# Kernel optimization log

Hardware: AMD Instinct MI355X
Metric: run time of the kernel (lower is better)

## Reference

```python
import jax, jax.numpy as jnp
import numpy as np

N_NODES = 100000
N_EDGES = 1600000
D_IN = 128
D_HID = 128
N_LAYERS = 3


def setup_inputs() -> dict:
    key = jax.random.key(0)
    k1, k2, k3, k4 = jax.random.split(key, 4)
    x = jax.random.normal(k1, (N_NODES, D_IN), dtype=jnp.float32)
    edge_index = jax.random.randint(k2, (2, N_EDGES), 0, N_NODES, dtype=jnp.int64)
    # Glorot-ish scale for stability across 3 layers
    Ws = jax.random.normal(k3, (N_LAYERS, D_IN, D_HID), dtype=jnp.float32) * (1.0 / np.sqrt(D_IN))
    bs = jax.random.normal(k4, (N_LAYERS, D_HID), dtype=jnp.float32) * 0.01
    return {"x": x, "edge_index": edge_index, "Ws": Ws, "bs": bs}


def _gcn_conv(x, row, col, deg_inv_sqrt, W, b, n_nodes):
    # Linear transform first (PyG GCNConv), then gather-normalize-scatter.
    h = x @ W                                        # [N, D]
    norm = deg_inv_sqrt[row] * deg_inv_sqrt[col]     # [E+N] (self-loops included)
    msg = h[row] * norm[:, None]                     # gather + scale, [E+N, D]
    out = jax.ops.segment_sum(msg, col, num_segments=n_nodes)  # scatter-add
    return out + b


def reference(x, edge_index, Ws, bs):
    n = x.shape[0]
    # add self-loops once (same for every layer)
    loop = jnp.arange(n, dtype=edge_index.dtype)
    row = jnp.concatenate([edge_index[0], loop])
    col = jnp.concatenate([edge_index[1], loop])
    # symmetric normalization: deg over target nodes (incl. self-loops)
    deg = jax.ops.segment_sum(jnp.ones_like(col, dtype=x.dtype), col, num_segments=n)
    deg_inv_sqrt = jnp.where(deg > 0, jax.lax.rsqrt(jnp.maximum(deg, 1.0)), 0.0)
    h = x
    for i in range(Ws.shape[0]):
        h = jax.nn.relu(_gcn_conv(h, row, col, deg_inv_sqrt, Ws[i], bs[i], n))
    return h
```

## Files before the change

### kernel.cpp

```cpp
#include <hip/hip_runtime.h>
#include <hip/hip_bf16.h>

#define NN 100000
#define NROWS 100032
#define NE 1600000
#define DD 128
#define NBUK 196
#define F1_BLOCKS 256
#define F3_BLOCKS 256

typedef unsigned short ushort_t;
typedef unsigned int uint_t;
typedef __attribute__((ext_vector_type(8))) short bf16x8;
typedef __attribute__((ext_vector_type(4))) float f32x4;

__device__ __forceinline__ ushort_t bf16rne(float f) {
    uint_t u = __float_as_uint(f);
    u += 0x7FFF + ((u >> 16) & 1);
    return (ushort_t)(u >> 16);
}
__device__ __forceinline__ float bfLo(uint_t u) { return __uint_as_float(u << 16); }
__device__ __forceinline__ float bfHi(uint_t u) { return __uint_as_float(u & 0xFFFF0000u); }


__global__ __launch_bounds__(256) void f1_bucket_count(const int* __restrict__ col,
                                                       int* __restrict__ bukCount) {
    __shared__ int hist[NBUK];
    for (int t = threadIdx.x; t < NBUK; t += 256) hist[t] = 0;
    __syncthreads();
    const int epb = (NE + F1_BLOCKS - 1) / F1_BLOCKS;
    const int e0 = blockIdx.x * epb;
    const int e1 = min(e0 + epb, NE);
    for (int e = e0 + threadIdx.x; e < e1; e += 256)
        atomicAdd(&hist[col[e] >> 9], 1);
    __syncthreads();
    for (int t = threadIdx.x; t < NBUK; t += 256)
        if (hist[t]) atomicAdd(&bukCount[t], hist[t]);
}

__global__ void f2_bucket_scan(const int* __restrict__ bukCount,
                               int* __restrict__ bukBase,
                               int* __restrict__ bukCursor,
                               int* __restrict__ offsets) {
    __shared__ int s[256];
    const int t = threadIdx.x;
    int v = (t < NBUK) ? bukCount[t] : 0;
    s[t] = v;
    __syncthreads();
    for (int off = 1; off < 256; off <<= 1) {
        int tmp = (t >= off) ? s[t - off] : 0;
        __syncthreads();
        s[t] += tmp;
        __syncthreads();
    }
    int excl = s[t] - v;
    if (t < NBUK) { bukBase[t] = excl; bukCursor[t] = excl; }
    if (t == 255) { bukBase[NBUK] = s[255]; offsets[NN] = s[255]; }
}

__global__ __launch_bounds__(256) void f3_scatter(const int* __restrict__ row,
                                                  const int* __restrict__ col,
                                                  int* __restrict__ bukCursor,
                                                  int* __restrict__ ebuf) {
    __shared__ int hist[4][NBUK];
    __shared__ int base[4][NBUK];
    const int t = threadIdx.x;
    const int w = t >> 6;
    const int lane = t & 63;
    for (int i = t; i < 4 * NBUK; i += 256) (&hist[0][0])[i] = 0;
    __syncthreads();
    const int epb = (NE + F3_BLOCKS - 1) / F3_BLOCKS;
    const int e0 = blockIdx.x * epb;
    const int e1 = min(e0 + epb, NE);
    const int wepb = (e1 - e0 + 3) >> 2;
    const int we0 = e0 + w * wepb;
    const int we1 = min(we0 + wepb, e1);
    for (int e = we0 + lane; e < we1; e += 64)
        atomicAdd(&hist[w][col[e] >> 9], 1);
    __syncthreads();
    if (t < NBUK) {
        int h0 = hist[0][t], h1 = hist[1][t], h2 = hist[2][t], h3 = hist[3][t];
        int tot = h0 + h1 + h2 + h3;
        int g = tot ? atomicAdd(&bukCursor[t], tot) : 0;
        base[0][t] = g; base[1][t] = g + h0;
        base[2][t] = g + h0 + h1; base[3][t] = g + h0 + h1 + h2;
        hist[0][t] = 0; hist[1][t] = 0; hist[2][t] = 0; hist[3][t] = 0;
    }
    __syncthreads();
    for (int e = we0 + lane; e < we1; e += 64) {
        int c = col[e];
        int b = c >> 9;
        int r = atomicAdd(&hist[w][b], 1);
        ebuf[base[w][b] + r] = (row[e] << 9) | (c & 511);
    }
}

__global__ __launch_bounds__(256) void f4_finalize(const int* __restrict__ ebuf,
                                                   const int* __restrict__ bukBase,
                                                   int* __restrict__ offsets,
                                                   float* __restrict__ dis,
                                                   int* __restrict__ csr_src) {
    __shared__ int cnt[512];
    __shared__ int cur[512];
    __shared__ int s[256];
    const int t = threadIdx.x;
    const int colBase = blockIdx.x << 9;
    const int ncols = min(512, NN - colBase);
    cnt[t] = 0; cnt[t + 256] = 0;
    __syncthreads();
    const int eb0 = bukBase[blockIdx.x];
    const int eb1 = bukBase[blockIdx.x + 1];
    for (int e = eb0 + t; e < eb1; e += 256)
        atomicAdd(&cnt[ebuf[e] & 511], 1);
    __syncthreads();
    const int c0 = cnt[2 * t], c1 = cnt[2 * t + 1];
    const int psum = c0 + c1;
    s[t] = psum;
    __syncthreads();
    for (int off = 1; off < 256; off <<= 1) {
        int tmp = (t >= off) ? s[t - off] : 0;
        __syncthreads();
        s[t] += tmp;
        __syncthreads();
    }
    const int exclPair = s[t] - psum;
    const int g0 = eb0 + exclPair;
    const int g1 = g0 + c0;
    cur[2 * t] = g0; cur[2 * t + 1] = g1;
    if (2 * t < ncols)     { offsets[colBase + 2 * t]     = g0; dis[colBase + 2 * t]     = rsqrtf((float)(c0 + 1)); }
    if (2 * t + 1 < ncols) { offsets[colBase + 2 * t + 1] = g1; dis[colBase + 2 * t + 1] = rsqrtf((float)(c1 + 1)); }
    __syncthreads();
    for (int e = eb0 + t; e < eb1; e += 256) {
        int pc = ebuf[e];
        int p = atomicAdd(&cur[pc & 511], 1);
        csr_src[p] = pc >> 9;
    }
}


__global__ __launch_bounds__(256) void wt_kernel(const float* __restrict__ Ws,
                                                 ushort_t* __restrict__ wT) {
    int idx = blockIdx.x * 256 + threadIdx.x;
    if (idx >= 3 * 128 * 16) return;
    int l = idx >> 11;
    int r = idx & 2047;
    int c = r >> 4;
    int kc = r & 15;
    const float* w = Ws + l * 16384;
    ushort_t tmp[8];
#pragma unroll
    for (int e = 0; e < 8; ++e)
        tmp[e] = bf16rne(w[(kc * 8 + e) * 128 + c]);
    *(uint4*)&wT[(size_t)l * 16384 + c * 128 + kc * 8] = *(uint4*)tmp;
}


template<bool XF32>
__global__ __launch_bounds__(256) void gemm_mfma(const void* __restrict__ Xv,
                                                 const ushort_t* __restrict__ wT,
                                                 const float* __restrict__ dis,
                                                 ushort_t* __restrict__ Y) {
    __shared__ short smem[128 * 136];
    {
        const uint4* src = (const uint4*)wT;
        int t = threadIdx.x;
#pragma unroll
        for (int i = 0; i < 8; ++i) {
            int idx = i * 256 + t;
            int rowc = idx >> 4;
            int kc = idx & 15;
            uint4 v = src[idx];
            *(uint4*)&smem[rowc * 136 + kc * 8] = v;
        }
    }
    __syncthreads();

    const int wave = threadIdx.x >> 6;
    const int lane = threadIdx.x & 63;
    const int m = lane & 15;
    const int kg = lane >> 4;
    const int r0 = blockIdx.x * 64 + wave * 16;
    const int rowA = min(r0 + m, NN - 1);

    f32x4 acc[8];
#pragma unroll
    for (int ct = 0; ct < 8; ++ct) acc[ct] = (f32x4){0.f, 0.f, 0.f, 0.f};

#pragma unroll
    for (int ks = 0; ks < 4; ++ks) {
        bf16x8 af;
        if (XF32) {
            const float* xp = (const float*)Xv + (size_t)rowA * DD + ks * 32 + kg * 8;
            float4 f0 = *(const float4*)xp;
            float4 f1 = *(const float4*)(xp + 4);
            af[0] = (short)bf16rne(f0.x); af[1] = (short)bf16rne(f0.y);
            af[2] = (short)bf16rne(f0.z); af[3] = (short)bf16rne(f0.w);
            af[4] = (short)bf16rne(f1.x); af[5] = (short)bf16rne(f1.y);
            af[6] = (short)bf16rne(f1.z); af[7] = (short)bf16rne(f1.w);
        } else {
            const ushort_t* xp = (const ushort_t*)Xv + (size_t)rowA * DD + ks * 32 + kg * 8;
            af = *(const bf16x8*)xp;
        }
#pragma unroll
        for (int ct = 0; ct < 8; ++ct) {
            bf16x8 bf = *(const bf16x8*)&smem[(ct * 16 + m) * 136 + ks * 32 + kg * 8];
            acc[ct] = __builtin_amdgcn_mfma_f32_16x16x32_bf16(af, bf, acc[ct], 0, 0, 0);
        }
    }

    __syncthreads();

    ushort_t* sl = (ushort_t*)smem;
    const int rbase = r0 + kg * 4;
    float dv[4];
#pragma unroll
    for (int rg = 0; rg < 4; ++rg) dv[rg] = dis[min(rbase + rg, NN - 1)];
#pragma unroll
    for (int ct = 0; ct < 8; ++ct) {
#pragma unroll
        for (int rg = 0; rg < 4; ++rg)
            sl[(wave * 16 + kg * 4 + rg) * 132 + ct * 16 + m] = bf16rne(acc[ct][rg] * dv[rg]);
    }

    const int lr = lane >> 2;
    const int q  = lane & 3;
    const int grow = r0 + lr;
    const ushort_t* rb = sl + (wave * 16 + lr) * 132 + q * 32;
    uint2 d0 = *(const uint2*)(rb + 0);
    uint2 d1 = *(const uint2*)(rb + 4);
    uint2 d2 = *(const uint2*)(rb + 8);
    uint2 d3 = *(const uint2*)(rb + 12);
    uint2 d4 = *(const uint2*)(rb + 16);
    uint2 d5 = *(const uint2*)(rb + 20);
    uint2 d6 = *(const uint2*)(rb + 24);
    uint2 d7 = *(const uint2*)(rb + 28);
    const bool ok = grow < NN;
    uint4 v0 = ok ? make_uint4(d0.x, d0.y, d1.x, d1.y) : make_uint4(0, 0, 0, 0);
    uint4 v1 = ok ? make_uint4(d2.x, d2.y, d3.x, d3.y) : make_uint4(0, 0, 0, 0);
    uint4 v2 = ok ? make_uint4(d4.x, d4.y, d5.x, d5.y) : make_uint4(0, 0, 0, 0);
    uint4 v3 = ok ? make_uint4(d6.x, d6.y, d7.x, d7.y) : make_uint4(0, 0, 0, 0);
    uint4* yp = (uint4*)&Y[(size_t)grow * DD + q * 32];
    yp[0] = v0; yp[1] = v1; yp[2] = v2; yp[3] = v3;
}


template<bool F32OUT>
__global__ __launch_bounds__(256) void agg_kernel(const uint_t* __restrict__ lin2,
                                                  const int* __restrict__ offsets,
                                                  const int* __restrict__ csr_src,
                                                  const float* __restrict__ dis,
                                                  const float* __restrict__ bias,
                                                  void* __restrict__ outv) {
    const int bid = blockIdx.x;
    const int xcd = bid & 7;
    const int h   = (xcd >> 2);
    const int g   = (bid >> 3) * 4 + (xcd & 3);
    const int w    = threadIdx.x >> 6;
    const int lane = threadIdx.x & 63;
    const int l32  = lane & 31;
    const int hi   = lane >> 5;
    const int v = g * 8 + w * 2 + hi;

    const int start = offsets[v];
    const int end   = offsets[v + 1];
    const int n     = end - start;
    const int nvm   = n < 32 ? n : 32;

    int idxv = NN;
    if (l32 < nvm) idxv = csr_src[start + l32];

    const int nv_other = __shfl(nvm, lane ^ 32);
    int kmax = nvm > nv_other ? nvm : nv_other;
    kmax = (kmax + 7) & ~7;

    const uint_t doff = (uint_t)(h * 32 + l32);
    const float dv = dis[v];
    uint_t self = lin2[((uint_t)v << 6) | doff];
    float2 b    = ((const float2*)bias)[doff];

    float accx = 0.f, accy = 0.f;
    const int sbase = (lane & 32);
    for (int k = 0; k < kmax; k += 8) {
        int s0 = __shfl(idxv, sbase + k + 0);
        int s1 = __shfl(idxv, sbase + k + 1);
        int s2 = __shfl(idxv, sbase + k + 2);
        int s3 = __shfl(idxv, sbase + k + 3);
        int s4 = __shfl(idxv, sbase + k + 4);
        int s5 = __shfl(idxv, sbase + k + 5);
        int s6 = __shfl(idxv, sbase + k + 6);
        int s7 = __shfl(idxv, sbase + k + 7);
        uint_t a0 = lin2[((uint_t)s0 << 6) | doff];
        uint_t a1 = lin2[((uint_t)s1 << 6) | doff];
        uint_t a2 = lin2[((uint_t)s2 << 6) | doff];
        uint_t a3 = lin2[((uint_t)s3 << 6) | doff];
        uint_t a4 = lin2[((uint_t)s4 << 6) | doff];
        uint_t a5 = lin2[((uint_t)s5 << 6) | doff];
        uint_t a6 = lin2[((uint_t)s6 << 6) | doff];
        uint_t a7 = lin2[((uint_t)s7 << 6) | doff];
        accx += bfLo(a0) + bfLo(a1) + bfLo(a2) + bfLo(a3)
              + bfLo(a4) + bfLo(a5) + bfLo(a6) + bfLo(a7);
        accy += bfHi(a0) + bfHi(a1) + bfHi(a2) + bfHi(a3)
              + bfHi(a4) + bfHi(a5) + bfHi(a6) + bfHi(a7);
    }
    for (int e = start + 32; e < end; ++e) {
        uint_t s = (uint_t)csr_src[e];
        uint_t a = lin2[(s << 6) | doff];
        accx += bfLo(a); accy += bfHi(a);
    }

    float rx = fmaxf(dv * (accx + bfLo(self)) + b.x, 0.f);
    float ry = fmaxf(dv * (accy + bfHi(self)) + b.y, 0.f);
    const size_t oidx = (size_t)v * 64 + doff;
    if (F32OUT) {
        float2 o = make_float2(rx, ry);
        __builtin_nontemporal_store(*(const double*)&o, (double*)((float2*)outv + oidx));
    } else {
        uint_t pk = (uint_t)bf16rne(rx) | ((uint_t)bf16rne(ry) << 16);
        __builtin_nontemporal_store(pk, (uint_t*)outv + oidx);
    }
}


extern "C" void kernel_launch(void* const* d_in, const int* in_sizes, int n_in,
                              void* d_out, int out_size, void* d_ws, size_t ws_size,
                              hipStream_t stream) {
    const float* x   = (const float*)d_in[0];
    const int*   ei  = (const int*)d_in[1];
    const float* Ws  = (const float*)d_in[2];
    const float* bs  = (const float*)d_in[3];

    const int* row = ei;
    const int* col = ei + NE;

    char* ws = (char*)d_ws;
    ushort_t* lin    = (ushort_t*)(ws + 0);
    int*   ebuf      = (int*)  (ws + 0);
    ushort_t* hb     = (ushort_t*)(ws + 25608192);
    float* dis       = (float*)(ws + 51208192);
    int*   offsets   = (int*)  (ws + 51608192);
    int*   csr_src   = (int*)  (ws + 52008208);
    int*   bukCount  = (int*)  (ws + 58408208);
    int*   bukBase   = (int*)  (ws + 58409008);
    int*   bukCursor = (int*)  (ws + 58409808);
    ushort_t* wT     = (ushort_t*)(ws + 58410608);

    hipMemsetAsync(bukCount, 0, NBUK * sizeof(int), stream);
    f1_bucket_count<<<F1_BLOCKS, 256, 0, stream>>>(col, bukCount);
    f2_bucket_scan<<<1, 256, 0, stream>>>(bukCount, bukBase, bukCursor, offsets);
    f3_scatter<<<F3_BLOCKS, 256, 0, stream>>>(row, col, bukCursor, ebuf);
    f4_finalize<<<NBUK, 256, 0, stream>>>(ebuf, bukBase, offsets, dis, csr_src);
    wt_kernel<<<24, 256, 0, stream>>>(Ws, wT);

    const int gemmGrid = NROWS / 64;
    const int aggGrid = (NN / 8) * 2;
    gemm_mfma<true><<<gemmGrid, 256, 0, stream>>>(x, wT, dis, lin);
    agg_kernel<false><<<aggGrid, 256, 0, stream>>>((const uint_t*)lin, offsets, csr_src, dis, bs, hb);
    gemm_mfma<false><<<gemmGrid, 256, 0, stream>>>(hb, wT + 16384, dis, lin);
    agg_kernel<false><<<aggGrid, 256, 0, stream>>>((const uint_t*)lin, offsets, csr_src, dis, bs + DD, hb);
    gemm_mfma<false><<<gemmGrid, 256, 0, stream>>>(hb, wT + 32768, dis, lin);
    agg_kernel<true><<<aggGrid, 256, 0, stream>>>((const uint_t*)lin, offsets, csr_src, dis, bs + 2 * DD, d_out);
}
```

Baseline: 293.2 us.

## Store GEMM output as feature-sliced planes and aggregate one slice per block

The GEMM epilogue now writes its bf16 output into 8 column planes of 16 features each (32 bytes per row per plane), with nontemporal stores. The aggregation kernel assigns each block one plane, selected by the low 3 bits of the block id, and processes 4 nodes per block. Within a wave, 8 edges are gathered in parallel, each by 8 lanes, and a shuffle reduction combines them; the self-loop is handled as an extra edge. The aim is to keep each XCD's gathers within one plane for better L2 locality. The cost is smaller 32-byte gathers and more blocks per launch.

```diff
diff --git a/kernel.cpp b/kernel.cpp
--- a/kernel.cpp
+++ b/kernel.cpp
@@ -11,6 +11,7 @@
 
 typedef unsigned short ushort_t;
 typedef unsigned int uint_t;
+typedef unsigned long long uint64_t_;
 typedef __attribute__((ext_vector_type(8))) short bf16x8;
 typedef __attribute__((ext_vector_type(4))) float f32x4;
 
@@ -222,101 +223,69 @@
             sl[(wave * 16 + kg * 4 + rg) * 132 + ct * 16 + m] = bf16rne(acc[ct][rg] * dv[rg]);
     }
 
-    const int lr = lane >> 2;
-    const int q  = lane & 3;
-    const int grow = r0 + lr;
-    const ushort_t* rb = sl + (wave * 16 + lr) * 132 + q * 32;
-    uint2 d0 = *(const uint2*)(rb + 0);
-    uint2 d1 = *(const uint2*)(rb + 4);
-    uint2 d2 = *(const uint2*)(rb + 8);
-    uint2 d3 = *(const uint2*)(rb + 12);
-    uint2 d4 = *(const uint2*)(rb + 16);
-    uint2 d5 = *(const uint2*)(rb + 20);
-    uint2 d6 = *(const uint2*)(rb + 24);
-    uint2 d7 = *(const uint2*)(rb + 28);
+    const int i = threadIdx.x >> 2;
+    const int q = threadIdx.x & 3;
+    const int grow = blockIdx.x * 64 + i;
     const bool ok = grow < NN;
-    uint4 v0 = ok ? make_uint4(d0.x, d0.y, d1.x, d1.y) : make_uint4(0, 0, 0, 0);
-    uint4 v1 = ok ? make_uint4(d2.x, d2.y, d3.x, d3.y) : make_uint4(0, 0, 0, 0);
-    uint4 v2 = ok ? make_uint4(d4.x, d4.y, d5.x, d5.y) : make_uint4(0, 0, 0, 0);
-    uint4 v3 = ok ? make_uint4(d6.x, d6.y, d7.x, d7.y) : make_uint4(0, 0, 0, 0);
-    uint4* yp = (uint4*)&Y[(size_t)grow * DD + q * 32];
-    yp[0] = v0; yp[1] = v1; yp[2] = v2; yp[3] = v3;
+    const ushort_t* rb = sl + i * 132;
+    uint64_t_* lp2 = (uint64_t_*)Y;
+#pragma unroll
+    for (int s = 0; s < 8; ++s) {
+        const uint_t* p = (const uint_t*)(rb + s * 16 + q * 4);
+        uint64_t_ d = (uint64_t_)p[0] | ((uint64_t_)p[1] << 32);
+        uint64_t_ z = ok ? d : 0ull;
+        __builtin_nontemporal_store(z, &lp2[((size_t)s * NROWS + grow) * 4 + q]);
+    }
 }
 
 
 template<bool F32OUT>
-__global__ __launch_bounds__(256) void agg_kernel(const uint_t* __restrict__ lin2,
+__global__ __launch_bounds__(256) void agg_kernel(const uint_t* __restrict__ lin_planes,
                                                   const int* __restrict__ offsets,
                                                   const int* __restrict__ csr_src,
                                                   const float* __restrict__ dis,
                                                   const float* __restrict__ bias,
                                                   void* __restrict__ outv) {
     const int bid = blockIdx.x;
-    const int xcd = bid & 7;
-    const int h   = (xcd >> 2);
-    const int g   = (bid >> 3) * 4 + (xcd & 3);
+    const int s   = bid & 7;
+    const int g   = bid >> 3;
     const int w    = threadIdx.x >> 6;
     const int lane = threadIdx.x & 63;
-    const int l32  = lane & 31;
-    const int hi   = lane >> 5;
-    const int v = g * 8 + w * 2 + hi;
+    const int es   = lane >> 3;
+    const int u    = lane & 7;
+    const int v = g * 4 + w;
 
     const int start = offsets[v];
-    const int end   = offsets[v + 1];
-    const int n     = end - start;
-    const int nvm   = n < 32 ? n : 32;
-
-    int idxv = NN;
-    if (l32 < nvm) idxv = csr_src[start + l32];
-
-    const int nv_other = __shfl(nvm, lane ^ 32);
-    int kmax = nvm > nv_other ? nvm : nv_other;
-    kmax = (kmax + 7) & ~7;
-
-    const uint_t doff = (uint_t)(h * 32 + l32);
+    const int deg   = offsets[v + 1] - start;
+
+    const uint_t* plane = lin_planes + (size_t)s * (NROWS * 8);
+
+    float accx = 0.f, accy = 0.f;
+    for (int k = 0; k <= deg; k += 8) {
+        int j = k + es;
+        int cj = j < deg ? j : 0;
+        int src = __builtin_nontemporal_load(&csr_src[start + cj]);
+        src = j < deg ? src : (j == deg ? v : NN);
+        uint_t a = plane[((uint_t)src << 3) + u];
+        accx += bfLo(a); accy += bfHi(a);
+    }
+    accx += __shfl_xor(accx, 8);  accy += __shfl_xor(accy, 8);
+    accx += __shfl_xor(accx, 16); accy += __shfl_xor(accy, 16);
+    accx += __shfl_xor(accx, 32); accy += __shfl_xor(accy, 32);
+
     const float dv = dis[v];
-    uint_t self = lin2[((uint_t)v << 6) | doff];
-    float2 b    = ((const float2*)bias)[doff];
-
-    float accx = 0.f, accy = 0.f;
-    const int sbase = (lane & 32);
-    for (int k = 0; k < kmax; k += 8) {
-        int s0 = __shfl(idxv, sbase + k + 0);
-        int s1 = __shfl(idxv, sbase + k + 1);
-        int s2 = __shfl(idxv, sbase + k + 2);
-        int s3 = __shfl(idxv, sbase + k + 3);
-        int s4 = __shfl(idxv, sbase + k + 4);
-        int s5 = __shfl(idxv, sbase + k + 5);
-        int s6 = __shfl(idxv, sbase + k + 6);
-        int s7 = __shfl(idxv, sbase + k + 7);
-        uint_t a0 = lin2[((uint_t)s0 << 6) | doff];
-        uint_t a1 = lin2[((uint_t)s1 << 6) | doff];
-        uint_t a2 = lin2[((uint_t)s2 << 6) | doff];
-        uint_t a3 = lin2[((uint_t)s3 << 6) | doff];
-        uint_t a4 = lin2[((uint_t)s4 << 6) | doff];
-        uint_t a5 = lin2[((uint_t)s5 << 6) | doff];
-        uint_t a6 = lin2[((uint_t)s6 << 6) | doff];
-        uint_t a7 = lin2[((uint_t)s7 << 6) | doff];
-        accx += bfLo(a0) + bfLo(a1) + bfLo(a2) + bfLo(a3)
-              + bfLo(a4) + bfLo(a5) + bfLo(a6) + bfLo(a7);
-        accy += bfHi(a0) + bfHi(a1) + bfHi(a2) + bfHi(a3)
-              + bfHi(a4) + bfHi(a5) + bfHi(a6) + bfHi(a7);
-    }
-    for (int e = start + 32; e < end; ++e) {
-        uint_t s = (uint_t)csr_src[e];
-        uint_t a = lin2[(s << 6) | doff];
-        accx += bfLo(a); accy += bfHi(a);
-    }
-
-    float rx = fmaxf(dv * (accx + bfLo(self)) + b.x, 0.f);
-    float ry = fmaxf(dv * (accy + bfHi(self)) + b.y, 0.f);
-    const size_t oidx = (size_t)v * 64 + doff;
-    if (F32OUT) {
-        float2 o = make_float2(rx, ry);
-        __builtin_nontemporal_store(*(const double*)&o, (double*)((float2*)outv + oidx));
-    } else {
-        uint_t pk = (uint_t)bf16rne(rx) | ((uint_t)bf16rne(ry) << 16);
-        __builtin_nontemporal_store(pk, (uint_t*)outv + oidx);
+    const float2 b = ((const float2*)bias)[s * 8 + u];
+    float rx = fmaxf(fmaf(dv, accx, b.x), 0.f);
+    float ry = fmaxf(fmaf(dv, accy, b.y), 0.f);
+    if (es == 0) {
+        const size_t oidx = (size_t)v * 64 + s * 8 + u;
+        if (F32OUT) {
+            float2 o = make_float2(rx, ry);
+            __builtin_nontemporal_store(*(const uint64_t_*)&o, (uint64_t_*)((float2*)outv + oidx));
+        } else {
+            uint_t pk = (uint_t)bf16rne(rx) | ((uint_t)bf16rne(ry) << 16);
+            __builtin_nontemporal_store(pk, (uint_t*)outv + oidx);
+        }
     }
 }
 
@@ -344,7 +313,7 @@
     int*   bukCursor = (int*)  (ws + 58409808);
     ushort_t* wT     = (ushort_t*)(ws + 58410608);
 
-    hipMemsetAsync(bukCount, 0, NBUK * sizeof(int), stream);
+    (void)hipMemsetAsync(bukCount, 0, NBUK * sizeof(int), stream);
     f1_bucket_count<<<F1_BLOCKS, 256, 0, stream>>>(col, bukCount);
     f2_bucket_scan<<<1, 256, 0, stream>>>(bukCount, bukBase, bukCursor, offsets);
     f3_scatter<<<F3_BLOCKS, 256, 0, stream>>>(row, col, bukCursor, ebuf);
@@ -352,7 +321,7 @@
     wt_kernel<<<24, 256, 0, stream>>>(Ws, wT);
 
     const int gemmGrid = NROWS / 64;
-    const int aggGrid = (NN / 8) * 2;
+    const int aggGrid = (NN / 4) * 8;
     gemm_mfma<true><<<gemmGrid, 256, 0, stream>>>(x, wT, dis, lin);
     agg_kernel<false><<<aggGrid, 256, 0, stream>>>((const uint_t*)lin, offsets, csr_src, dis, bs, hb);
     gemm_mfma<false><<<gemmGrid, 256, 0, stream>>>(hb, wT + 16384, dis, lin);
```

Result: slower. 1.019 ms (+247.4%).
